# Optimization experiments

Measured on AMD Instinct MI355X. Metric: run time of the kernel, lower is better.

Reference implementation:

```python
import jax, jax.numpy as jnp
import numpy as np

EPS = 1e-5  # BatchNorm2d default eps
PAD = 7     # width padding; conv-transpose equiv pad = k-1-p = 15-1-7 = 7


def _conv(x, w):
    # NCHW conv, kernel (O,I,1,T), stride 1, padding (0, PAD)
    return jax.lax.conv_general_dilated(
        x, w, window_strides=(1, 1), padding=((0, 0), (PAD, PAD)),
        dimension_numbers=('NCHW', 'OIHW', 'NCHW'))


def setup_inputs() -> dict:
    key = jax.random.key(0)
    ks = jax.random.split(key, 4)
    B, H, D = 32, 64, 256          # batch, electrodes, time (= patch_size = codebook dim)
    C, K, T = 16, 2048, 15         # channel_size, codebook size, temp_kernel
    x = jax.random.normal(ks[0], (B, 1, H, D), dtype=jnp.float32)
    # xavier_uniform_ for both convs (fan_in/fan_out from torch conv weight shapes)
    lim_e = float(np.sqrt(6.0 / (1 * T + C * T)))
    w_enc = jax.random.uniform(ks[1], (C, 1, 1, T), jnp.float32, -lim_e, lim_e)
    lim_d = float(np.sqrt(6.0 / (C * T + 1 * T)))
    # torch ConvTranspose2d weight layout: (in_ch=C, out_ch=1, 1, T)
    w_dec = jax.random.uniform(ks[2], (C, 1, 1, T), jnp.float32, -lim_d, lim_d)
    gamma = jnp.ones((C,), jnp.float32)   # BatchNorm2d weight
    beta = jnp.zeros((C,), jnp.float32)   # BatchNorm2d bias
    emb = jax.random.uniform(ks[3], (K, D), jnp.float32, -1.0 / K, 1.0 / K)
    return dict(x=x, w_enc=w_enc, gamma=gamma, beta=beta, emb=emb, w_dec=w_dec)


def reference(x, w_enc, gamma, beta, emb, w_dec):
    # ---- encode: Conv2d(1,C,(1,T),pad=(0,7),bias=False) + BatchNorm2d (train mode) ----
    z = _conv(x, w_enc)                                   # (B,C,H,D)
    m = z.mean(axis=(0, 2, 3), keepdims=True)
    v = z.var(axis=(0, 2, 3), keepdims=True)
    z_e = gamma[None, :, None, None] * (z - m) * jax.lax.rsqrt(v + EPS) \
        + beta[None, :, None, None]                       # (B,C,H,D)
    # ---- VQ: squared distance to each codeword over the time axis, argmin over K ----
    # dists[b,c,h,k] = sum_d (z_e[b,c,h,d] - emb[k,d])^2, via norm expansion (no (B,K,D,C,H) blowup)
    dots = jnp.einsum('bchd,kd->bchk', z_e, emb)
    dists = (z_e * z_e).sum(-1)[..., None] - 2.0 * dots + (emb * emb).sum(-1)
    latents = jnp.argmin(dists, axis=-1)                  # (B,C,H) int
    # ---- decode: embedding gather + ConvTranspose2d(C,1,(1,T),pad=(0,7)) + tanh ----
    z_q = emb[latents]                                    # (B,C,H,D)
    # stride-1 transposed conv == conv with channel-swapped, spatially-flipped kernel, pad k-1-p
    w_t = jnp.flip(jnp.transpose(w_dec, (1, 0, 2, 3)), axis=(2, 3))  # (1,C,1,T)
    x_tilde = jnp.tanh(_conv(z_q, w_t))                   # (B,1,H,D)
    return x_tilde, z_e, z_q
```

## Files before the change

### kernel.cpp

```cpp
#include <hip/hip_runtime.h>
#include <hip/hip_bf16.h>
#include <cstddef>
#include <cstdint>

#define B   32
#define C   16
#define H   64
#define D   256
#define K   2048
#define T   15
#define PAD 7
#define EPS 1e-5

#define BH      (B*H)
#define ROWS    (B*C*H)
#define N_PER_CH ((double)(B*H*D))
#define NC  8

typedef __attribute__((ext_vector_type(8))) short bf16x8;
typedef __attribute__((ext_vector_type(4))) float f32x4;

__device__ __forceinline__ void gload_lds16(const void* g, void* l) {
  __builtin_amdgcn_global_load_lds(
      (const __attribute__((address_space(1))) unsigned int*)g,
      (__attribute__((address_space(3))) unsigned int*)l, 16, 0, 0);
}

__global__ __launch_bounds__(256) void k0_fused(
    const float* __restrict__ x, const float* __restrict__ w,
    double* __restrict__ partial ,
    const float* __restrict__ emb, double* __restrict__ enorm,
    float* __restrict__ enormf, __hip_bfloat16* __restrict__ embB) {
  __shared__ __attribute__((aligned(16))) float xs[272];
  __shared__ float wsm[C*T];
  const int bh = blockIdx.x, tid = threadIdx.x;
  if (bh >= BH) {
    const int k = (bh - BH) * 4 + (tid >> 6);
    const int lane = tid & 63;
    const float4 ev = *(const float4*)(emb + ((size_t)k << 8) + lane*4);
    __hip_bfloat16 hb[4] = {__float2bfloat16(ev.x), __float2bfloat16(ev.y),
                            __float2bfloat16(ev.z), __float2bfloat16(ev.w)};
    *(int2*)(embB + ((size_t)k << 8) + lane*4) = *(const int2*)hb;
    double s = fma((double)ev.x, (double)ev.x,
               fma((double)ev.y, (double)ev.y,
               fma((double)ev.z, (double)ev.z,
                   (double)ev.w * (double)ev.w)));
#pragma unroll
    for (int off = 1; off < 64; off <<= 1) s += __shfl_xor(s, off, 64);
    if (lane == 0) { enorm[k] = s; enormf[k] = (float)s; }
    return;
  }
  const float* xrow = x + ((size_t)bh << 8);
  if (tid < C*T) wsm[tid] = w[tid];
  xs[tid] = (tid >= 7 && tid < 263) ? xrow[tid - 7] : 0.f;
  if (tid < 16) { int i = 256 + tid; xs[i] = (i < 263) ? xrow[i - 7] : 0.f; }
  __syncthreads();
  const int c = tid >> 4, s = tid & 15;
  float xr[32];
#pragma unroll
  for (int kq = 0; kq < 8; kq++)
    *(float4*)&xr[kq*4] = *(const float4*)&xs[s*16 + kq*4];
  float wv[T];
#pragma unroll
  for (int t = 0; t < T; t++) wv[t] = wsm[c*T + t];
  double sum = 0.0, sq = 0.0;
#pragma unroll
  for (int d0 = 0; d0 < 16; d0++) {
    double z = 0.0;
#pragma unroll
    for (int t = 0; t < T; t++) z = fma((double)wv[t], (double)xr[d0 + t], z);
    sum += z; sq = fma(z, z, sq);
  }
#pragma unroll
  for (int off = 1; off < 16; off <<= 1) {
    sum += __shfl_xor(sum, off, 64);
    sq  += __shfl_xor(sq,  off, 64);
  }
  if (s == 0) {
    partial[((size_t)c*BH + bh)*2 + 0] = sum;
    partial[((size_t)c*BH + bh)*2 + 1] = sq;
  }
}

__global__ __launch_bounds__(256) void k2_stats_final(
    const double* __restrict__ partial, const float* __restrict__ gamma,
    const float* __restrict__ beta, double* __restrict__ params) {
  __shared__ double rs[256], rq[256];
  const int c = blockIdx.x;
  const int tid = threadIdx.x;
  double s = 0.0, q = 0.0;
  for (int i = tid; i < BH; i += 256) {
    s += partial[((size_t)c*BH + i)*2 + 0];
    q += partial[((size_t)c*BH + i)*2 + 1];
  }
  rs[tid] = s; rq[tid] = q;
  __syncthreads();
  for (int off = 128; off; off >>= 1) {
    if (tid < off) { rs[tid] += rs[tid + off]; rq[tid] += rq[tid + off]; }
    __syncthreads();
  }
  if (tid == 0) {
    double m = rs[0] / N_PER_CH;
    double v = rq[0] / N_PER_CH - m * m;
    double a = (double)gamma[c] / sqrt(v + EPS);
    double b = (double)beta[c] - a * m;
    params[c*4+0] = m; params[c*4+1] = v; params[c*4+2] = a; params[c*4+3] = b;
  }
}

__global__ __launch_bounds__(256) void k1b_ze(
    const float* __restrict__ x, const float* __restrict__ w,
    const double* __restrict__ params, float* __restrict__ zE,
    __hip_bfloat16* __restrict__ zEb) {
  __shared__ __attribute__((aligned(16))) float xs[272];
  __shared__ float wsm[C*T];
  const int bh = blockIdx.x, tid = threadIdx.x;
  const int b = bh >> 6, h = bh & 63;
  const float* xrow = x + ((size_t)bh << 8);
  if (tid < C*T) wsm[tid] = w[tid];
  xs[tid] = (tid >= 7 && tid < 263) ? xrow[tid - 7] : 0.f;
  if (tid < 16) { int i = 256 + tid; xs[i] = (i < 263) ? xrow[i - 7] : 0.f; }
  __syncthreads();
  const int c = tid >> 4, s = tid & 15;
  float xr[32];
#pragma unroll
  for (int kq = 0; kq < 8; kq++)
    *(float4*)&xr[kq*4] = *(const float4*)&xs[s*16 + kq*4];
  float wv[T];
#pragma unroll
  for (int t = 0; t < T; t++) wv[t] = wsm[c*T + t];
  const double a = params[c*4+2], bb = params[c*4+3];
  float zf[16];
  __hip_bfloat16 zb[16];
#pragma unroll
  for (int d0 = 0; d0 < 16; d0++) {
    double z = 0.0;
#pragma unroll
    for (int t = 0; t < T; t++) z = fma((double)wv[t], (double)xr[d0 + t], z);
    double ze = fma(a, z, bb);
    zf[d0] = (float)ze;
    zb[d0] = __float2bfloat16(zf[d0]);
  }
  const size_t rbase = ((((size_t)b*C + c)*H + h) << 8) + s*16;
#pragma unroll
  for (int kq = 0; kq < 4; kq++)
    *(float4*)(zE + rbase + kq*4) = *(const float4*)&zf[kq*4];
  *(int4*)(zEb + rbase)     = *(const int4*)&zb[0];
  *(int4*)(zEb + rbase + 8) = *(const int4*)&zb[8];
}

__global__ __launch_bounds__(256, 2) void k4_mfma(
    const __hip_bfloat16* __restrict__ zEb, const __hip_bfloat16* __restrict__ embB,
    const float* __restrict__ enormf, int* __restrict__ cand ) {
  __shared__ __attribute__((aligned(16))) __hip_bfloat16 Ash[64][512];
  __shared__ __attribute__((aligned(16))) __hip_bfloat16 Bsh[2][8][512];

  const int tid  = threadIdx.x;
  const int w    = tid >> 6, lane = tid & 63;
  const int wr   = w >> 1,   wc   = w & 1;
  const int l15  = lane & 15, l4  = lane >> 4;
  const int mblk = blockIdx.x >> 1, nhalf = blockIdx.x & 1;
  const int row0 = mblk * 128;
  const int n0   = nhalf * 1024;

#pragma unroll
  for (int i = 0; i < 16; i++) {
    int f = w*16 + i;
    int kk = f >> 3, mf = f & 7;
    gload_lds16(zEb + (((size_t)(row0 + mf*16 + l15)) << 8) + kk*32 + l4*8,
                &Ash[kk*8 + mf][0]);
  }
  auto stageB = [&](int t) {
    const int slot = t & 1, nt = t >> 3, kk = t & 7;
#pragma unroll
    for (int j = 0; j < 2; j++) {
      int nf = w*2 + j;
      gload_lds16(embB + (((size_t)(n0 + nt*128 + nf*16 + l15)) << 8) + kk*32 + l4*8,
                  &Bsh[slot][nf][0]);
    }
  };
  stageB(0);
  asm volatile("s_waitcnt vmcnt(0) lgkmcnt(0)" ::: "memory");
  __builtin_amdgcn_sched_barrier(0);
  __builtin_amdgcn_s_barrier();

  unsigned t0[16], t1[16];
#pragma unroll
  for (int s = 0; s < 16; s++) { t0[s] = 0xFFFFFFFFu; t1[s] = 0xFFFFFFFFu; }

  f32x4 accA[4][4], accB[4][4];
  float enC0 = 0.f, enC1 = 0.f, enC2 = 0.f, enC3 = 0.f;
  float enP0 = 0.f, enP1 = 0.f, enP2 = 0.f, enP3 = 0.f;

  auto runphase = [&](f32x4 (&ACC)[4][4], f32x4 (&PRV)[4][4],
                      int ntbase, int pnt, bool dp) {
#pragma unroll
    for (int m = 0; m < 4; m++)
#pragma unroll
      for (int n = 0; n < 4; n++) ACC[m][n] = (f32x4){0.f, 0.f, 0.f, 0.f};

#pragma unroll
    for (int kk = 0; kk < 8; kk++) {
      const int t = ntbase*8 + kk;
      if (t) __builtin_amdgcn_s_barrier();
      if (t < 63) {
        stageB(t + 1);
        if (kk == 1) asm volatile("s_waitcnt vmcnt(6)" ::: "memory");
        else         asm volatile("s_waitcnt vmcnt(2)" ::: "memory");
      } else {
        asm volatile("s_waitcnt vmcnt(0)" ::: "memory");
      }
      __builtin_amdgcn_sched_barrier(0);
      __builtin_amdgcn_s_barrier();

      if (kk == 0) {
        enP0 = enC0; enP1 = enC1; enP2 = enC2; enP3 = enC3;
        enC0 = enormf[n0 + ntbase*128 + (wc*4 + 0)*16 + l15];
        enC1 = enormf[n0 + ntbase*128 + (wc*4 + 1)*16 + l15];
        enC2 = enormf[n0 + ntbase*128 + (wc*4 + 2)*16 + l15];
        enC3 = enormf[n0 + ntbase*128 + (wc*4 + 3)*16 + l15];
      }

      bf16x8 af[4], bfr[4];
#pragma unroll
      for (int m = 0; m < 4; m++)
        af[m] = *(const bf16x8*)&Ash[kk*8 + wr*4 + m][lane*8];
#pragma unroll
      for (int n = 0; n < 4; n++)
        bfr[n] = *(const bf16x8*)&Bsh[t & 1][wc*4 + n][lane*8];
#pragma unroll
      for (int m = 0; m < 4; m++)
#pragma unroll
        for (int n = 0; n < 4; n++)
          ACC[m][n] = __builtin_amdgcn_mfma_f32_16x16x32_bf16(af[m], bfr[n], ACC[m][n], 0, 0, 0);

      if (dp) {
        const int n = kk >> 1, hf = kk & 1;
        const float pen = (n == 0) ? enP0 : (n == 1) ? enP1 : (n == 2) ? enP2 : enP3;
        const int pcol = n0 + pnt*128 + (wc*4 + n)*16 + l15;
#pragma unroll
        for (int mm = 0; mm < 2; mm++) {
          const int m = hf*2 + mm;
#pragma unroll
          for (int r = 0; r < 4; r++) {
            const float cv = fmaf(-2.f, PRV[m][n][r], pen);
            unsigned u = __float_as_uint(cv);
            unsigned key = u ^ ((unsigned)((int)u >> 31) | 0x80000000u);
            key = (key & 0xFFFFF800u) | (unsigned)pcol;
            const int s = m*4 + r;
            unsigned mx = key > t0[s] ? key : t0[s];
            t0[s] = key < t0[s] ? key : t0[s];
            t1[s] = mx < t1[s] ? mx : t1[s];
          }
        }
      }
    }
  };

  for (int nt = 0; nt < 8; nt += 2) {
    runphase(accA, accB, nt,     nt - 1, nt > 0);
    runphase(accB, accA, nt + 1, nt,     true);
  }
#pragma unroll
  for (int kk = 0; kk < 8; kk++) {
    const int n = kk >> 1, hf = kk & 1;
    const float pen = (n == 0) ? enC0 : (n == 1) ? enC1 : (n == 2) ? enC2 : enC3;
    const int pcol = n0 + 7*128 + (wc*4 + n)*16 + l15;
#pragma unroll
    for (int mm = 0; mm < 2; mm++) {
      const int m = hf*2 + mm;
#pragma unroll
      for (int r = 0; r < 4; r++) {
        const float cv = fmaf(-2.f, accB[m][n][r], pen);
        unsigned u = __float_as_uint(cv);
        unsigned key = u ^ ((unsigned)((int)u >> 31) | 0x80000000u);
        key = (key & 0xFFFFF800u) | (unsigned)pcol;
        const int s = m*4 + r;
        unsigned mx = key > t0[s] ? key : t0[s];
        t0[s] = key < t0[s] ? key : t0[s];
        t1[s] = mx < t1[s] ? mx : t1[s];
      }
    }
  }

  __syncthreads();
  unsigned* KeyM = (unsigned*)&Ash[0][0];
  const int tk = wc*16 + l15;
#pragma unroll
  for (int s = 0; s < 16; s++) {
    const int r = wr*64 + (s >> 2)*16 + l4*4 + (s & 3);
    KeyM[r*65 + tk*2 + 0] = t0[s];
    KeyM[r*65 + tk*2 + 1] = t1[s];
  }
  __syncthreads();
  if (tid < 128) {
    unsigned bk[4];
#pragma unroll
    for (int j = 0; j < 4; j++) bk[j] = 0xFFFFFFFFu;
    for (int e = 0; e < 64; e++) {
      unsigned v = KeyM[tid*65 + e];
      if (v < bk[3]) {
        int j = 3;
        while (j > 0 && v < bk[j-1]) { bk[j] = bk[j-1]; j--; }
        bk[j] = v;
      }
    }
    int* cr = cand + ((size_t)(row0 + tid)) * NC + nhalf*4;
#pragma unroll
    for (int j = 0; j < 4; j++) cr[j] = (int)(bk[j] & 2047u);
  }
}

__global__ __launch_bounds__(256) void k6_rescore(
    const float* __restrict__ zE, const float* __restrict__ emb,
    const double* __restrict__ enorm, const int* __restrict__ cand,
    double* __restrict__ rscV, int* __restrict__ rscK) {
  const int wv = threadIdx.x >> 6, lane = threadIdx.x & 63;
  const size_t row = (size_t)blockIdx.x * 4 + wv;
  const int j = lane >> 3, q = lane & 7;
  const int k = cand[row * NC + j];
  const float* er = emb + ((size_t)k << 8);
  const float* zr = zE + (row << 8);
  double a0 = 0.0, a1 = 0.0, a2 = 0.0, a3 = 0.0;
#pragma unroll
  for (int it = 0; it < 8; it++) {
    const int e0 = it*32 + q*4;
    const float4 ev = *(const float4*)(er + e0);
    const float4 zv = *(const float4*)(zr + e0);
    a0 = fma((double)ev.x, (double)zv.x, a0);
    a1 = fma((double)ev.y, (double)zv.y, a1);
    a2 = fma((double)ev.z, (double)zv.z, a2);
    a3 = fma((double)ev.w, (double)zv.w, a3);
  }
  double dot = (a0 + a1) + (a2 + a3);
  dot += __shfl_xor(dot, 1, 64);
  dot += __shfl_xor(dot, 2, 64);
  dot += __shfl_xor(dot, 4, 64);
  double cv = enorm[k] - 2.0 * dot;
  int bk = k;
#pragma unroll
  for (int off = 8; off < 32; off <<= 1) {
    double ocv = __shfl_xor(cv, off, 64);
    int    okk = __shfl_xor(bk, off, 64);
    if (ocv < cv || (ocv == cv && okk < bk)) { cv = ocv; bk = okk; }
  }
  if ((lane & 31) == 0) {
    rscV[row*2 + (lane >> 5)] = cv;
    rscK[row*2 + (lane >> 5)] = bk;
  }
}

__global__ __launch_bounds__(256) void k7_decode(
    const float* __restrict__ emb, const double* __restrict__ rscV,
    const int* __restrict__ rscK, const float* __restrict__ wdec,
    float* __restrict__ zq, float* __restrict__ xt) {
  __shared__ __attribute__((aligned(16))) float zs[C][272];
  __shared__ __attribute__((aligned(16))) float part[4][256];
  __shared__ float wt[C*T];
  __shared__ int bkS[C];
  const int bh = blockIdx.x, b = bh >> 6, h = bh & 63;
  const int tid = threadIdx.x;

  if (tid < C) {
    const size_t rid = ((size_t)b*C + tid)*H + h;
    const double cv0 = rscV[rid*2 + 0], cv1 = rscV[rid*2 + 1];
    const int    k0  = rscK[rid*2 + 0], k1  = rscK[rid*2 + 1];
    bkS[tid] = (cv1 < cv0 || (cv1 == cv0 && k1 < k0)) ? k1 : k0;
  }
  if (tid < C*T) {
    int c = tid / T, t = tid % T;
    wt[c*T + t] = wdec[c*T + (T-1-t)];
  }
  __syncthreads();

  for (int i2 = tid; i2 < C*D; i2 += 256) {
    int c = i2 >> 8, dd = i2 & 255;
    float v = emb[((size_t)bkS[c] << 8) + dd];
    zs[c][dd + PAD] = v;
    zq[((((size_t)b*C + c)*H + h) << 8) + dd] = v;
  }
  { int jj = tid & 15, c = tid >> 4;
    int pos = (jj < 7) ? jj : (256 + PAD + (jj - 7));
    zs[c][pos] = 0.f; }
  __syncthreads();

  const int dg = tid & 63, cg = tid >> 6;
  float f[20];
  float oo[4] = {0.f, 0.f, 0.f, 0.f};
#pragma unroll
  for (int ci = 0; ci < 4; ci++) {
    const int c = cg*4 + ci;
#pragma unroll
    for (int kq = 0; kq < 5; kq++)
      *(float4*)&f[kq*4] = *(const float4*)&zs[c][dg*4 + kq*4];
#pragma unroll
    for (int jj = 0; jj < 4; jj++)
#pragma unroll
      for (int t = 0; t < T; t++)
        oo[jj] = fmaf(wt[c*T + t], f[jj + t], oo[jj]);
  }
  *(float4*)&part[cg][dg*4] = make_float4(oo[0], oo[1], oo[2], oo[3]);
  __syncthreads();
  float r = part[0][tid] + part[1][tid] + part[2][tid] + part[3][tid];
  xt[((size_t)bh << 8) + tid] = tanhf(r);
}

extern "C" void kernel_launch(void* const* d_in, const int* in_sizes, int n_in,
                              void* d_out, int out_size, void* d_ws, size_t ws_size,
                              hipStream_t stream) {
  const float* x     = (const float*)d_in[0];
  const float* w_enc = (const float*)d_in[1];
  const float* gamma = (const float*)d_in[2];
  const float* beta  = (const float*)d_in[3];
  const float* emb   = (const float*)d_in[4];
  const float* w_dec = (const float*)d_in[5];

  float* out = (float*)d_out;
  float* xt = out;
  float* zE = out + (size_t)B*H*D;
  float* zq = out + (size_t)B*H*D + (size_t)B*C*H*D;

  char* ws = (char*)d_ws;
  double* partial = (double*)(ws);
  double* params  = (double*)(ws + 524288);
  double* enorm   = (double*)(ws + 524800);
  float*  enormf  = (float*) (ws + 541184);
  int*    cand    = (int*)   (ws + 549376);
  double* rscV    = (double*)(ws + 1597952);
  int*    rscK    = (int*)   (ws + 2122240);
  __hip_bfloat16* zEb  = (__hip_bfloat16*)(ws + 2384384);
  __hip_bfloat16* embB = (__hip_bfloat16*)(ws + 19161600);

  k0_fused<<<BH + 512, 256, 0, stream>>>(x, w_enc, partial, emb, enorm, enormf, embB);
  k2_stats_final<<<C, 256, 0, stream>>>(partial, gamma, beta, params);
  k1b_ze<<<BH, 256, 0, stream>>>(x, w_enc, params, zE, zEb);
  k4_mfma<<<512, 256, 0, stream>>>(zEb, embB, enormf, cand);
  k6_rescore<<<ROWS/4, 256, 0, stream>>>(zE, emb, enorm, cand, rscV, rscK);
  k7_decode<<<BH, 256, 0, stream>>>(emb, rscV, rscK, w_dec, zq, xt);
}
```

Baseline: 131.2 us.

## Restructure MFMA B-staging per wave column, add setprio, move z_q gather into rescore

In the MFMA argmin kernel, each wave now stages only the B fragments it consumes (its column half), so each wave waits on its own loads rather than a full block barrier. It also raises wave priority around the MFMA burst. Separately, the rescore kernel now finishes the full 8-candidate argmin and writes the selected codeword row straight into z_q, so the decode kernel just reads z_q and the rscV/rscK round trip goes away. The cost is duplicated B loads across waves that share a column, plus a re-read of z_q in decode. The block barrier ordering around the double buffer also changes, so there is some risk of LDS hazards.

```diff
diff --git a/kernel.cpp b/kernel.cpp
--- a/kernel.cpp
+++ b/kernel.cpp
@@ -173,14 +173,14 @@
   auto stageB = [&](int t) {
     const int slot = t & 1, nt = t >> 3, kk = t & 7;
 #pragma unroll
-    for (int j = 0; j < 2; j++) {
-      int nf = w*2 + j;
+    for (int n = 0; n < 4; n++) {
+      const int nf = wc*4 + n;
       gload_lds16(embB + (((size_t)(n0 + nt*128 + nf*16 + l15)) << 8) + kk*32 + l4*8,
                   &Bsh[slot][nf][0]);
     }
   };
   stageB(0);
-  asm volatile("s_waitcnt vmcnt(0) lgkmcnt(0)" ::: "memory");
+  asm volatile("s_waitcnt vmcnt(4)" ::: "memory");
   __builtin_amdgcn_sched_barrier(0);
   __builtin_amdgcn_s_barrier();
 
@@ -202,16 +202,16 @@
 #pragma unroll
     for (int kk = 0; kk < 8; kk++) {
       const int t = ntbase*8 + kk;
-      if (t) __builtin_amdgcn_s_barrier();
-      if (t < 63) {
-        stageB(t + 1);
-        if (kk == 1) asm volatile("s_waitcnt vmcnt(6)" ::: "memory");
-        else         asm volatile("s_waitcnt vmcnt(2)" ::: "memory");
-      } else {
-        asm volatile("s_waitcnt vmcnt(0)" ::: "memory");
+      if (t) {
+        asm volatile("s_waitcnt lgkmcnt(0)" ::: "memory");
+        __builtin_amdgcn_sched_barrier(0);
+        __builtin_amdgcn_s_barrier();
       }
+      if (t < 63) stageB(t + 1);
+      if (t == 63)      asm volatile("s_waitcnt vmcnt(0)" ::: "memory");
+      else if (kk == 1) asm volatile("s_waitcnt vmcnt(8)" ::: "memory");
+      else              asm volatile("s_waitcnt vmcnt(4)" ::: "memory");
       __builtin_amdgcn_sched_barrier(0);
-      __builtin_amdgcn_s_barrier();
 
       if (kk == 0) {
         enP0 = enC0; enP1 = enC1; enP2 = enC2; enP3 = enC3;
@@ -228,11 +228,13 @@
 #pragma unroll
       for (int n = 0; n < 4; n++)
         bfr[n] = *(const bf16x8*)&Bsh[t & 1][wc*4 + n][lane*8];
+      __builtin_amdgcn_s_setprio(1);
 #pragma unroll
       for (int m = 0; m < 4; m++)
 #pragma unroll
         for (int n = 0; n < 4; n++)
           ACC[m][n] = __builtin_amdgcn_mfma_f32_16x16x32_bf16(af[m], bfr[n], ACC[m][n], 0, 0, 0);
+      __builtin_amdgcn_s_setprio(0);
 
       if (dp) {
         const int n = kk >> 1, hf = kk & 1;
@@ -314,7 +316,7 @@
 __global__ __launch_bounds__(256) void k6_rescore(
     const float* __restrict__ zE, const float* __restrict__ emb,
     const double* __restrict__ enorm, const int* __restrict__ cand,
-    double* __restrict__ rscV, int* __restrict__ rscK) {
+    float* __restrict__ zq) {
   const int wv = threadIdx.x >> 6, lane = threadIdx.x & 63;
   const size_t row = (size_t)blockIdx.x * 4 + wv;
   const int j = lane >> 3, q = lane & 7;
@@ -339,45 +341,31 @@
   double cv = enorm[k] - 2.0 * dot;
   int bk = k;
 #pragma unroll
-  for (int off = 8; off < 32; off <<= 1) {
+  for (int off = 8; off < 64; off <<= 1) {
     double ocv = __shfl_xor(cv, off, 64);
     int    okk = __shfl_xor(bk, off, 64);
     if (ocv < cv || (ocv == cv && okk < bk)) { cv = ocv; bk = okk; }
   }
-  if ((lane & 31) == 0) {
-    rscV[row*2 + (lane >> 5)] = cv;
-    rscK[row*2 + (lane >> 5)] = bk;
-  }
+  const float4 ew = *(const float4*)(emb + ((size_t)bk << 8) + lane*4);
+  *(float4*)(zq + (row << 8) + lane*4) = ew;
 }
 
 __global__ __launch_bounds__(256) void k7_decode(
-    const float* __restrict__ emb, const double* __restrict__ rscV,
-    const int* __restrict__ rscK, const float* __restrict__ wdec,
-    float* __restrict__ zq, float* __restrict__ xt) {
+    const float* __restrict__ zq, const float* __restrict__ wdec,
+    float* __restrict__ xt) {
   __shared__ __attribute__((aligned(16))) float zs[C][272];
   __shared__ __attribute__((aligned(16))) float part[4][256];
   __shared__ float wt[C*T];
-  __shared__ int bkS[C];
   const int bh = blockIdx.x, b = bh >> 6, h = bh & 63;
   const int tid = threadIdx.x;
 
-  if (tid < C) {
-    const size_t rid = ((size_t)b*C + tid)*H + h;
-    const double cv0 = rscV[rid*2 + 0], cv1 = rscV[rid*2 + 1];
-    const int    k0  = rscK[rid*2 + 0], k1  = rscK[rid*2 + 1];
-    bkS[tid] = (cv1 < cv0 || (cv1 == cv0 && k1 < k0)) ? k1 : k0;
-  }
   if (tid < C*T) {
     int c = tid / T, t = tid % T;
     wt[c*T + t] = wdec[c*T + (T-1-t)];
   }
-  __syncthreads();
-
   for (int i2 = tid; i2 < C*D; i2 += 256) {
     int c = i2 >> 8, dd = i2 & 255;
-    float v = emb[((size_t)bkS[c] << 8) + dd];
-    zs[c][dd + PAD] = v;
-    zq[((((size_t)b*C + c)*H + h) << 8) + dd] = v;
+    zs[c][dd + PAD] = zq[((((size_t)b*C + c)*H + h) << 8) + dd];
   }
   { int jj = tid & 15, c = tid >> 4;
     int pos = (jj < 7) ? jj : (256 + PAD + (jj - 7));
@@ -426,15 +414,13 @@
   double* enorm   = (double*)(ws + 524800);
   float*  enormf  = (float*) (ws + 541184);
   int*    cand    = (int*)   (ws + 549376);
-  double* rscV    = (double*)(ws + 1597952);
-  int*    rscK    = (int*)   (ws + 2122240);
-  __hip_bfloat16* zEb  = (__hip_bfloat16*)(ws + 2384384);
-  __hip_bfloat16* embB = (__hip_bfloat16*)(ws + 19161600);
+  __hip_bfloat16* zEb  = (__hip_bfloat16*)(ws + 1597952);
+  __hip_bfloat16* embB = (__hip_bfloat16*)(ws + 18375168);
 
   k0_fused<<<BH + 512, 256, 0, stream>>>(x, w_enc, partial, emb, enorm, enormf, embB);
   k2_stats_final<<<C, 256, 0, stream>>>(partial, gamma, beta, params);
   k1b_ze<<<BH, 256, 0, stream>>>(x, w_enc, params, zE, zEb);
   k4_mfma<<<512, 256, 0, stream>>>(zEb, embB, enormf, cand);
-  k6_rescore<<<ROWS/4, 256, 0, stream>>>(zE, emb, enorm, cand, rscV, rscK);
-  k7_decode<<<BH, 256, 0, stream>>>(emb, rscV, rscK, w_dec, zq, xt);
-}
+  k6_rescore<<<ROWS/4, 256, 0, stream>>>(zE, emb, enorm, cand, zq);
+  k7_decode<<<BH, 256, 0, stream>>>(zq, w_dec, xt);
+}
```

Measured after the change: 166.5 us. +26.9%, slower.
